# Performance work log

Measured on AMD Instinct MI355X. Metric: run time of the kernel, lower is better.

The kernel has to match this reference:

```python
import jax, jax.numpy as jnp
import numpy as np

ALPHA, BETA, GAMMA = 2.0, 2.0, 1.0
EPS = 1e-8  # torch F.cosine_similarity eps
B, T, D = 64, 1024, 256


def setup_inputs() -> dict:
    key = jax.random.key(0)
    k1, k2, k3 = jax.random.split(key, 3)
    f_v = jax.random.normal(k1, (B, T, D), dtype=jnp.float32)
    f_a = jax.random.normal(k2, (B, T, D), dtype=jnp.float32)
    labels = jax.random.randint(k3, (B,), 0, 2, dtype=jnp.int64)
    return {"f_v": f_v, "f_a": f_a, "labels": labels}


def _normalize(x):
    n = jnp.sqrt(jnp.sum(x * x, axis=-1, keepdims=True))
    return x / jnp.maximum(n, EPS)


def reference(f_v, f_a, labels):
    b, t, _ = f_v.shape
    vn = _normalize(f_v)  # [B,T,D]
    an = _normalize(f_a)  # [B,T,D]

    # --- per-timestep aligned-pair term ---
    cos_bt = jnp.sum(vn * an, axis=-1)  # [B,T] cosine sim
    d_bt = 1.0 - cos_bt                  # cosine distance
    pos_mask = (labels == 0).astype(f_v.dtype)[:, None]  # [B,1]
    neg_mask = 1.0 - pos_mask
    loss_pos = ALPHA * jnp.sum(d_bt * pos_mask)
    cnt_pos = jnp.sum(pos_mask) * t
    loss_neg = BETA * jnp.sum((1.0 - d_bt) * neg_mask)  # (1-d) == cos
    cnt_neg = jnp.sum(neg_mask) * t

    # --- cross-sample term: for i != j, (1 - mean_t d_ij) = mean_t cos(v_i_t, a_j_t) ---
    cross_cos = jnp.einsum('itd,jtd->ij', vn, an) / t  # [B,B] mean over T
    offdiag = 1.0 - jnp.eye(b, dtype=f_v.dtype)
    loss_neg = loss_neg + GAMMA * jnp.sum(cross_cos * offdiag)
    cnt_neg = cnt_neg + b * (b - 1)

    loss = jnp.where(cnt_pos > 0, loss_pos / jnp.maximum(cnt_pos, 1.0), 0.0)
    loss = loss + jnp.where(cnt_neg > 0, loss_neg / jnp.maximum(cnt_neg, 1.0), 0.0)
    return loss
```

## Files before the change

### kernel.cpp

```cpp
#include <hip/hip_runtime.h>

constexpr int Bn = 64;
constexpr int Tn = 1024;
constexpr int Dn = 256;

constexpr int TPB  = 256;
constexpr int NBLK = Tn;

using short8 = __attribute__((ext_vector_type(8))) short;
using f32x16 = __attribute__((ext_vector_type(16))) float;

__device__ __forceinline__ float dot4(const float4& a, const float4& b) {
    return a.x * b.x + a.y * b.y + a.z * b.z + a.w * b.w;
}

__device__ __forceinline__ unsigned int bfbits(float x) {
    unsigned int u = __builtin_bit_cast(unsigned int, x);
    return (u + 0x7FFFu + ((u >> 16) & 1u)) >> 16;
}
__device__ __forceinline__ unsigned int pack_bf2(float lo, float hi) {
    return bfbits(lo) | (bfbits(hi) << 16);
}

__global__ __launch_bounds__(TPB, 4)
void cmfm_main(const float* __restrict__ fv, const float* __restrict__ fa,
               const int* __restrict__ labels, float* __restrict__ acc)
{
    __shared__ __align__(16) unsigned int Vb[Bn * 64];
    __shared__ __align__(16) unsigned int Ab[Bn * 64];
    __shared__ float rvs[Bn], ras[Bn];
    __shared__ float wred[3][TPB / 64];

    const int tid  = threadIdx.x;
    const int row  = tid >> 2;
    const int q    = tid & 3;
    const int lane = tid & 63;
    const int wave = tid >> 6;

    const int lab = labels[row];
    const float4* __restrict__ fv4 = reinterpret_cast<const float4*>(fv);
    const float4* __restrict__ fa4 = reinterpret_cast<const float4*>(fa);

    const int t = blockIdx.x;
    const size_t base = ((size_t)row * Tn + t) * (Dn / 4);

    const int i0   = (wave >> 1) * 32;
    const int j0   = (wave & 1) * 32;
    const int mrow = lane & 31;
    const int half = lane >> 5;
    const int rsx  = mrow & 15;
    const unsigned vrb = (unsigned)(i0 + mrow) * 64;
    const unsigned arb = (unsigned)(j0 + mrow) * 64;

    const int wsx = row & 15;
    const unsigned wrb = (unsigned)row * 64;

    f32x16 C;
    #pragma unroll
    for (int r = 0; r < 16; ++r) C[r] = 0.f;

    float sqv = 0.f, sqa = 0.f, dva = 0.f;
    float rv = 0.f, ra = 0.f;

    #pragma unroll
    for (int h = 0; h < 2; ++h) {
        float4 v4[8], a4[8];
        #pragma unroll
        for (int k = 0; k < 8; ++k) v4[k] = fv4[base + q + 4 * (8 * h + k)];
        #pragma unroll
        for (int k = 0; k < 8; ++k) a4[k] = fa4[base + q + 4 * (8 * h + k)];

        #pragma unroll
        for (int k = 0; k < 8; ++k) {
            sqv += dot4(v4[k], v4[k]);
            sqa += dot4(a4[k], a4[k]);
            dva += dot4(v4[k], a4[k]);
        }

        #pragma unroll
        for (int k = 0; k < 8; ++k) {
            const int d4l  = q + 4 * k;
            const int slot = d4l >> 1;
            const unsigned idx = wrb + (unsigned)(((slot ^ wsx) << 2) + (d4l & 1) * 2);
            uint2 pv, pa;
            pv.x = pack_bf2(v4[k].x, v4[k].y); pv.y = pack_bf2(v4[k].z, v4[k].w);
            pa.x = pack_bf2(a4[k].x, a4[k].y); pa.y = pack_bf2(a4[k].z, a4[k].w);
            *reinterpret_cast<uint2*>(&Vb[idx]) = pv;
            *reinterpret_cast<uint2*>(&Ab[idx]) = pa;
        }

        if (h == 1) {
            sqv += __shfl_xor(sqv, 1); sqv += __shfl_xor(sqv, 2);
            sqa += __shfl_xor(sqa, 1); sqa += __shfl_xor(sqa, 2);
            dva += __shfl_xor(dva, 1); dva += __shfl_xor(dva, 2);
            rv = 1.f / fmaxf(sqrtf(sqv), 1e-8f);
            ra = 1.f / fmaxf(sqrtf(sqa), 1e-8f);
            if (q == 0) { rvs[row] = rv; ras[row] = ra; }
        }
        __syncthreads();

        #pragma unroll
        for (int s = 0; s < 8; ++s) {
            const int slotl = s * 2 + half;
            const short8 av = *reinterpret_cast<const short8*>(&Vb[vrb + ((slotl ^ rsx) << 2)]);
            const short8 bv = *reinterpret_cast<const short8*>(&Ab[arb + ((slotl ^ rsx) << 2)]);
            C = __builtin_amdgcn_mfma_f32_32x32x16_bf16(av, bv, C, 0, 0, 0);
        }
        if (h == 0) __syncthreads();
    }

    float pos_acc = 0.f, neg_acc = 0.f;
    if (q == 0) {
        const float cosd = dva * rv * ra;
        if (lab == 0) pos_acc = 1.f - cosd;
        else          neg_acc = cosd;
    }

    const float raj = ras[j0 + mrow];
    float od = 0.f;
    #pragma unroll
    for (int r = 0; r < 16; ++r) {
        const int ri = (r & 3) + 8 * (r >> 2) + 4 * half;
        float c = C[r];
        if (i0 == j0 && ri == mrow) c = 0.f;
        od += rvs[i0 + ri] * raj * c;
    }

    #pragma unroll
    for (int off = 1; off < 64; off <<= 1) {
        pos_acc += __shfl_xor(pos_acc, off);
        neg_acc += __shfl_xor(neg_acc, off);
        od      += __shfl_xor(od, off);
    }
    if (lane == 0) { wred[0][wave] = pos_acc; wred[1][wave] = neg_acc; wred[2][wave] = od; }
    __syncthreads();
    if (tid == 0) {
        float p = 0.f, n = 0.f, o = 0.f;
        #pragma unroll
        for (int w = 0; w < TPB / 64; ++w) { p += wred[0][w]; n += wred[1][w]; o += wred[2][w]; }
        atomicAdd(&acc[0],  p);
        atomicAdd(&acc[16], n);
        atomicAdd(&acc[32], o);
    }
}

__global__ void cmfm_final(const int* __restrict__ labels, const float* __restrict__ acc,
                           float* __restrict__ out) {
    if (threadIdx.x == 0) {
        int npos = 0;
        for (int i = 0; i < Bn; ++i) npos += (labels[i] == 0);
        const float pos_sum   = acc[0];
        const float neg_sum   = acc[16];
        const float cross_sum = acc[32];

        const float cnt_pos = (float)npos * (float)Tn;
        const float cnt_neg = (float)(Bn - npos) * (float)Tn + (float)Bn * (float)(Bn - 1);

        float loss = 0.f;
        if (npos > 0) loss += 2.0f * pos_sum / cnt_pos;
        loss += (2.0f * neg_sum + 1.0f * cross_sum / (float)Tn) / cnt_neg;
        out[0] = loss;
    }
}

extern "C" void kernel_launch(void* const* d_in, const int* in_sizes, int n_in,
                              void* d_out, int out_size, void* d_ws, size_t ws_size,
                              hipStream_t stream) {
    const float* fv     = (const float*)d_in[0];
    const float* fa     = (const float*)d_in[1];
    const int*   labels = (const int*)d_in[2];
    float* acc = (float*)d_ws;
    float* out = (float*)d_out;

    hipMemsetAsync(acc, 0, 64 * sizeof(float), stream);
    cmfm_main<<<NBLK, TPB, 0, stream>>>(fv, fa, labels, acc);
    cmfm_final<<<1, 64, 0, stream>>>(labels, acc, out);
}
```

Measured before the change: 161.0 us.

## Software-pipeline D-chunk loads and fold final reduction into main kernel

Splits the D dimension into four 64-wide chunks with double-buffered register prefetch, so global loads of the next chunk overlap the bf16 packing and MFMA work on the current one. Shared staging buffers are halved and the swizzle is adjusted to match. The separate finalize kernel is removed: the last block, found through an atomic ticket counter, computes the loss, and the positive-label count is derived inside each block. This trades one kernel launch for more barriers per block and a threadfence plus atomic counter.

Result: slower. 198.5 us (+23.3%).

```diff
diff --git a/kernel.cpp b/kernel.cpp
--- a/kernel.cpp
+++ b/kernel.cpp
@@ -24,12 +24,13 @@
 
 __global__ __launch_bounds__(TPB, 4)
 void cmfm_main(const float* __restrict__ fv, const float* __restrict__ fa,
-               const int* __restrict__ labels, float* __restrict__ acc)
+               const int* __restrict__ labels, float* __restrict__ acc,
+               float* __restrict__ out)
 {
-    __shared__ __align__(16) unsigned int Vb[Bn * 64];
-    __shared__ __align__(16) unsigned int Ab[Bn * 64];
+    __shared__ __align__(16) unsigned int Vb[Bn * 32];
+    __shared__ __align__(16) unsigned int Ab[Bn * 32];
     __shared__ float rvs[Bn], ras[Bn];
-    __shared__ float wred[3][TPB / 64];
+    __shared__ float wred[4][TPB / 64];
 
     const int tid  = threadIdx.x;
     const int row  = tid >> 2;
@@ -48,12 +49,12 @@
     const int j0   = (wave & 1) * 32;
     const int mrow = lane & 31;
     const int half = lane >> 5;
-    const int rsx  = mrow & 15;
-    const unsigned vrb = (unsigned)(i0 + mrow) * 64;
-    const unsigned arb = (unsigned)(j0 + mrow) * 64;
+    const int rsx  = mrow & 7;
+    const unsigned vrb = (unsigned)(i0 + mrow) * 32;
+    const unsigned arb = (unsigned)(j0 + mrow) * 32;
 
-    const int wsx = row & 15;
-    const unsigned wrb = (unsigned)row * 64;
+    const int wsx = row & 7;
+    const unsigned wrb = (unsigned)row * 32;
 
     f32x16 C;
     #pragma unroll
@@ -62,34 +63,43 @@
     float sqv = 0.f, sqa = 0.f, dva = 0.f;
     float rv = 0.f, ra = 0.f;
 
+    float4 va[2][4], ab4[2][4];
+
     #pragma unroll
-    for (int h = 0; h < 2; ++h) {
-        float4 v4[8], a4[8];
-        #pragma unroll
-        for (int k = 0; k < 8; ++k) v4[k] = fv4[base + q + 4 * (8 * h + k)];
-        #pragma unroll
-        for (int k = 0; k < 8; ++k) a4[k] = fa4[base + q + 4 * (8 * h + k)];
+    for (int k = 0; k < 4; ++k) va[0][k] = fv4[base + q + 4 * k];
+    #pragma unroll
+    for (int k = 0; k < 4; ++k) ab4[0][k] = fa4[base + q + 4 * k];
 
-        #pragma unroll
-        for (int k = 0; k < 8; ++k) {
-            sqv += dot4(v4[k], v4[k]);
-            sqa += dot4(a4[k], a4[k]);
-            dva += dot4(v4[k], a4[k]);
+    #pragma unroll
+    for (int qq = 0; qq < 4; ++qq) {
+        const int cur = qq & 1;
+        const int nxt = cur ^ 1;
+
+        if (qq < 3) {
+            #pragma unroll
+            for (int k = 0; k < 4; ++k) va[nxt][k]  = fv4[base + (qq + 1) * 16 + q + 4 * k];
+            #pragma unroll
+            for (int k = 0; k < 4; ++k) ab4[nxt][k] = fa4[base + (qq + 1) * 16 + q + 4 * k];
         }
 
         #pragma unroll
-        for (int k = 0; k < 8; ++k) {
+        for (int k = 0; k < 4; ++k) {
+            const float4 v = va[cur][k];
+            const float4 a = ab4[cur][k];
+            sqv += dot4(v, v);
+            sqa += dot4(a, a);
+            dva += dot4(v, a);
             const int d4l  = q + 4 * k;
             const int slot = d4l >> 1;
             const unsigned idx = wrb + (unsigned)(((slot ^ wsx) << 2) + (d4l & 1) * 2);
             uint2 pv, pa;
-            pv.x = pack_bf2(v4[k].x, v4[k].y); pv.y = pack_bf2(v4[k].z, v4[k].w);
-            pa.x = pack_bf2(a4[k].x, a4[k].y); pa.y = pack_bf2(a4[k].z, a4[k].w);
+            pv.x = pack_bf2(v.x, v.y); pv.y = pack_bf2(v.z, v.w);
+            pa.x = pack_bf2(a.x, a.y); pa.y = pack_bf2(a.z, a.w);
             *reinterpret_cast<uint2*>(&Vb[idx]) = pv;
             *reinterpret_cast<uint2*>(&Ab[idx]) = pa;
         }
 
-        if (h == 1) {
+        if (qq == 3) {
             sqv += __shfl_xor(sqv, 1); sqv += __shfl_xor(sqv, 2);
             sqa += __shfl_xor(sqa, 1); sqa += __shfl_xor(sqa, 2);
             dva += __shfl_xor(dva, 1); dva += __shfl_xor(dva, 2);
@@ -100,20 +110,20 @@
         __syncthreads();
 
         #pragma unroll
-        for (int s = 0; s < 8; ++s) {
+        for (int s = 0; s < 4; ++s) {
             const int slotl = s * 2 + half;
             const short8 av = *reinterpret_cast<const short8*>(&Vb[vrb + ((slotl ^ rsx) << 2)]);
             const short8 bv = *reinterpret_cast<const short8*>(&Ab[arb + ((slotl ^ rsx) << 2)]);
             C = __builtin_amdgcn_mfma_f32_32x32x16_bf16(av, bv, C, 0, 0, 0);
         }
-        if (h == 0) __syncthreads();
+        __syncthreads();
     }
 
-    float pos_acc = 0.f, neg_acc = 0.f;
+    float pos_acc = 0.f, neg_acc = 0.f, npos_i = 0.f;
     if (q == 0) {
         const float cosd = dva * rv * ra;
-        if (lab == 0) pos_acc = 1.f - cosd;
-        else          neg_acc = cosd;
+        if (lab == 0) { pos_acc = 1.f - cosd; npos_i = 1.f; }
+        else          { neg_acc = cosd; }
     }
 
     const float raj = ras[j0 + mrow];
@@ -131,35 +141,39 @@
         pos_acc += __shfl_xor(pos_acc, off);
         neg_acc += __shfl_xor(neg_acc, off);
         od      += __shfl_xor(od, off);
+        npos_i  += __shfl_xor(npos_i, off);
     }
-    if (lane == 0) { wred[0][wave] = pos_acc; wred[1][wave] = neg_acc; wred[2][wave] = od; }
+    if (lane == 0) {
+        wred[0][wave] = pos_acc; wred[1][wave] = neg_acc;
+        wred[2][wave] = od;      wred[3][wave] = npos_i;
+    }
     __syncthreads();
+
     if (tid == 0) {
-        float p = 0.f, n = 0.f, o = 0.f;
+        float p = 0.f, n = 0.f, o = 0.f, npf = 0.f;
         #pragma unroll
-        for (int w = 0; w < TPB / 64; ++w) { p += wred[0][w]; n += wred[1][w]; o += wred[2][w]; }
+        for (int w = 0; w < TPB / 64; ++w) {
+            p += wred[0][w]; n += wred[1][w]; o += wred[2][w]; npf += wred[3][w];
+        }
         atomicAdd(&acc[0],  p);
         atomicAdd(&acc[16], n);
         atomicAdd(&acc[32], o);
-    }
-}
-
-__global__ void cmfm_final(const int* __restrict__ labels, const float* __restrict__ acc,
-                           float* __restrict__ out) {
-    if (threadIdx.x == 0) {
-        int npos = 0;
-        for (int i = 0; i < Bn; ++i) npos += (labels[i] == 0);
-        const float pos_sum   = acc[0];
-        const float neg_sum   = acc[16];
-        const float cross_sum = acc[32];
-
-        const float cnt_pos = (float)npos * (float)Tn;
-        const float cnt_neg = (float)(Bn - npos) * (float)Tn + (float)Bn * (float)(Bn - 1);
-
-        float loss = 0.f;
-        if (npos > 0) loss += 2.0f * pos_sum / cnt_pos;
-        loss += (2.0f * neg_sum + 1.0f * cross_sum / (float)Tn) / cnt_neg;
-        out[0] = loss;
+        __threadfence();
+        int* ctr = reinterpret_cast<int*>(acc) + 48;
+        const int old = atomicAdd(ctr, 1);
+        if (old == NBLK - 1) {
+            __threadfence();
+            const float pos_sum   = atomicAdd(&acc[0],  0.f);
+            const float neg_sum   = atomicAdd(&acc[16], 0.f);
+            const float cross_sum = atomicAdd(&acc[32], 0.f);
+            const int   np        = (int)(npf + 0.5f);
+            const float cnt_pos = (float)np * (float)Tn;
+            const float cnt_neg = (float)(Bn - np) * (float)Tn + (float)Bn * (float)(Bn - 1);
+            float loss = 0.f;
+            if (np > 0) loss += 2.0f * pos_sum / cnt_pos;
+            loss += (2.0f * neg_sum + 1.0f * cross_sum / (float)Tn) / cnt_neg;
+            out[0] = loss;
+        }
     }
 }
 
@@ -173,6 +187,5 @@
     float* out = (float*)d_out;
 
     hipMemsetAsync(acc, 0, 64 * sizeof(float), stream);
-    cmfm_main<<<NBLK, TPB, 0, stream>>>(fv, fa, labels, acc);
-    cmfm_final<<<1, 64, 0, stream>>>(labels, acc, out);
+    cmfm_main<<<NBLK, TPB, 0, stream>>>(fv, fa, labels, acc, out);
 }
```

## Feed MFMA directly from registers with one-wave blocks per quadrant

Applied to the files above, without the earlier changes.

Each block becomes a single wave that handles one 32x32 quadrant of the cross-sample matrix at one timestep. It loads fp32 rows straight into registers, packs them to bf16 and feeds the MFMA without the shared-memory staging and barriers. Norms are exchanged with shuffles instead of LDS, and atomics are spread over 64 bins that the final kernel reduces. The cost is redundant global reads: each row is loaded by two quadrant blocks, doubling read traffic, which may rely on L2 hits.

New measurement: 272.9 us. 1.69x slower.

```diff
diff --git a/kernel.cpp b/kernel.cpp
--- a/kernel.cpp
+++ b/kernel.cpp
@@ -4,8 +4,10 @@
 constexpr int Tn = 1024;
 constexpr int Dn = 256;
 
-constexpr int TPB  = 256;
-constexpr int NBLK = Tn;
+constexpr int TPB   = 64;
+constexpr int QUADS = 4;
+constexpr int NBLK  = Tn * QUADS;
+constexpr int NBIN  = 64;
 
 using short8 = __attribute__((ext_vector_type(8))) short;
 using f32x16 = __attribute__((ext_vector_type(16))) float;
@@ -26,139 +28,108 @@
 void cmfm_main(const float* __restrict__ fv, const float* __restrict__ fa,
                const int* __restrict__ labels, float* __restrict__ acc)
 {
-    __shared__ __align__(16) unsigned int Vb[Bn * 64];
-    __shared__ __align__(16) unsigned int Ab[Bn * 64];
-    __shared__ float rvs[Bn], ras[Bn];
-    __shared__ float wred[3][TPB / 64];
+    const int lane = threadIdx.x;
+    const int bid  = blockIdx.x;
 
-    const int tid  = threadIdx.x;
-    const int row  = tid >> 2;
-    const int q    = tid & 3;
-    const int lane = tid & 63;
-    const int wave = tid >> 6;
-
-    const int lab = labels[row];
-    const float4* __restrict__ fv4 = reinterpret_cast<const float4*>(fv);
-    const float4* __restrict__ fa4 = reinterpret_cast<const float4*>(fa);
-
-    const int t = blockIdx.x;
-    const size_t base = ((size_t)row * Tn + t) * (Dn / 4);
-
-    const int i0   = (wave >> 1) * 32;
-    const int j0   = (wave & 1) * 32;
+    const int lid  = (bid & 7) * (NBLK / 8) + (bid >> 3);
+    const int t    = lid >> 2;
+    const int quad = lid & 3;
+    const int i0   = (quad >> 1) * 32;
+    const int j0   = (quad & 1) * 32;
     const int mrow = lane & 31;
     const int half = lane >> 5;
-    const int rsx  = mrow & 15;
-    const unsigned vrb = (unsigned)(i0 + mrow) * 64;
-    const unsigned arb = (unsigned)(j0 + mrow) * 64;
+    const bool diag = (i0 == j0);
 
-    const int wsx = row & 15;
-    const unsigned wrb = (unsigned)row * 64;
+    const float* __restrict__ vrow = fv + ((size_t)(i0 + mrow) * Tn + t) * Dn + 8 * half;
+    const float* __restrict__ arow = fa + ((size_t)(j0 + mrow) * Tn + t) * Dn + 8 * half;
 
     f32x16 C;
     #pragma unroll
     for (int r = 0; r < 16; ++r) C[r] = 0.f;
 
     float sqv = 0.f, sqa = 0.f, dva = 0.f;
-    float rv = 0.f, ra = 0.f;
 
     #pragma unroll
-    for (int h = 0; h < 2; ++h) {
-        float4 v4[8], a4[8];
-        #pragma unroll
-        for (int k = 0; k < 8; ++k) v4[k] = fv4[base + q + 4 * (8 * h + k)];
-        #pragma unroll
-        for (int k = 0; k < 8; ++k) a4[k] = fa4[base + q + 4 * (8 * h + k)];
+    for (int s = 0; s < 16; ++s) {
+        const float4 v0 = *reinterpret_cast<const float4*>(vrow + 16 * s);
+        const float4 v1 = *reinterpret_cast<const float4*>(vrow + 16 * s + 4);
+        const float4 a0 = *reinterpret_cast<const float4*>(arow + 16 * s);
+        const float4 a1 = *reinterpret_cast<const float4*>(arow + 16 * s + 4);
 
-        #pragma unroll
-        for (int k = 0; k < 8; ++k) {
-            sqv += dot4(v4[k], v4[k]);
-            sqa += dot4(a4[k], a4[k]);
-            dva += dot4(v4[k], a4[k]);
-        }
+        sqv += dot4(v0, v0) + dot4(v1, v1);
+        sqa += dot4(a0, a0) + dot4(a1, a1);
+        if (diag) dva += dot4(v0, a0) + dot4(v1, a1);
 
-        #pragma unroll
-        for (int k = 0; k < 8; ++k) {
-            const int d4l  = q + 4 * k;
-            const int slot = d4l >> 1;
-            const unsigned idx = wrb + (unsigned)(((slot ^ wsx) << 2) + (d4l & 1) * 2);
-            uint2 pv, pa;
-            pv.x = pack_bf2(v4[k].x, v4[k].y); pv.y = pack_bf2(v4[k].z, v4[k].w);
-            pa.x = pack_bf2(a4[k].x, a4[k].y); pa.y = pack_bf2(a4[k].z, a4[k].w);
-            *reinterpret_cast<uint2*>(&Vb[idx]) = pv;
-            *reinterpret_cast<uint2*>(&Ab[idx]) = pa;
-        }
+        union { short8 s8; uint4 u4; } av, bv;
+        av.u4.x = pack_bf2(v0.x, v0.y); av.u4.y = pack_bf2(v0.z, v0.w);
+        av.u4.z = pack_bf2(v1.x, v1.y); av.u4.w = pack_bf2(v1.z, v1.w);
+        bv.u4.x = pack_bf2(a0.x, a0.y); bv.u4.y = pack_bf2(a0.z, a0.w);
+        bv.u4.z = pack_bf2(a1.x, a1.y); bv.u4.w = pack_bf2(a1.z, a1.w);
 
-        if (h == 1) {
-            sqv += __shfl_xor(sqv, 1); sqv += __shfl_xor(sqv, 2);
-            sqa += __shfl_xor(sqa, 1); sqa += __shfl_xor(sqa, 2);
-            dva += __shfl_xor(dva, 1); dva += __shfl_xor(dva, 2);
-            rv = 1.f / fmaxf(sqrtf(sqv), 1e-8f);
-            ra = 1.f / fmaxf(sqrtf(sqa), 1e-8f);
-            if (q == 0) { rvs[row] = rv; ras[row] = ra; }
-        }
-        __syncthreads();
-
-        #pragma unroll
-        for (int s = 0; s < 8; ++s) {
-            const int slotl = s * 2 + half;
-            const short8 av = *reinterpret_cast<const short8*>(&Vb[vrb + ((slotl ^ rsx) << 2)]);
-            const short8 bv = *reinterpret_cast<const short8*>(&Ab[arb + ((slotl ^ rsx) << 2)]);
-            C = __builtin_amdgcn_mfma_f32_32x32x16_bf16(av, bv, C, 0, 0, 0);
-        }
-        if (h == 0) __syncthreads();
+        C = __builtin_amdgcn_mfma_f32_32x32x16_bf16(av.s8, bv.s8, C, 0, 0, 0);
     }
 
-    float pos_acc = 0.f, neg_acc = 0.f;
-    if (q == 0) {
+    sqv += __shfl_xor(sqv, 32);
+    sqa += __shfl_xor(sqa, 32);
+    const float rv = 1.f / fmaxf(sqrtf(sqv), 1e-8f);
+    const float ra = 1.f / fmaxf(sqrtf(sqa), 1e-8f);
+
+    float pos = 0.f, neg = 0.f;
+    if (diag) {
+        dva += __shfl_xor(dva, 32);
         const float cosd = dva * rv * ra;
-        if (lab == 0) pos_acc = 1.f - cosd;
-        else          neg_acc = cosd;
+        const int lab = labels[i0 + mrow];
+        if (half == 0) {
+            if (lab == 0) pos = 1.f - cosd;
+            else          neg = cosd;
+        }
     }
 
-    const float raj = ras[j0 + mrow];
     float od = 0.f;
     #pragma unroll
     for (int r = 0; r < 16; ++r) {
         const int ri = (r & 3) + 8 * (r >> 2) + 4 * half;
+        const float rvi = __shfl(rv, ri);
         float c = C[r];
-        if (i0 == j0 && ri == mrow) c = 0.f;
-        od += rvs[i0 + ri] * raj * c;
+        if (diag && ri == mrow) c = 0.f;
+        od += rvi * ra * c;
     }
 
     #pragma unroll
     for (int off = 1; off < 64; off <<= 1) {
-        pos_acc += __shfl_xor(pos_acc, off);
-        neg_acc += __shfl_xor(neg_acc, off);
-        od      += __shfl_xor(od, off);
+        pos += __shfl_xor(pos, off);
+        neg += __shfl_xor(neg, off);
+        od  += __shfl_xor(od, off);
     }
-    if (lane == 0) { wred[0][wave] = pos_acc; wred[1][wave] = neg_acc; wred[2][wave] = od; }
-    __syncthreads();
-    if (tid == 0) {
-        float p = 0.f, n = 0.f, o = 0.f;
-        #pragma unroll
-        for (int w = 0; w < TPB / 64; ++w) { p += wred[0][w]; n += wred[1][w]; o += wred[2][w]; }
-        atomicAdd(&acc[0],  p);
-        atomicAdd(&acc[16], n);
-        atomicAdd(&acc[32], o);
+    if (lane == 0) {
+        float* bin = acc + (size_t)(bid & (NBIN - 1)) * 4;
+        atomicAdd(bin + 0, pos);
+        atomicAdd(bin + 1, neg);
+        atomicAdd(bin + 2, od);
     }
 }
 
 __global__ void cmfm_final(const int* __restrict__ labels, const float* __restrict__ acc,
                            float* __restrict__ out) {
-    if (threadIdx.x == 0) {
-        int npos = 0;
-        for (int i = 0; i < Bn; ++i) npos += (labels[i] == 0);
-        const float pos_sum   = acc[0];
-        const float neg_sum   = acc[16];
-        const float cross_sum = acc[32];
-
-        const float cnt_pos = (float)npos * (float)Tn;
-        const float cnt_neg = (float)(Bn - npos) * (float)Tn + (float)Bn * (float)(Bn - 1);
-
+    const int l = threadIdx.x;
+    float p = acc[l * 4 + 0];
+    float n = acc[l * 4 + 1];
+    float o = acc[l * 4 + 2];
+    float npf = (labels[l] == 0) ? 1.f : 0.f;
+    #pragma unroll
+    for (int off = 1; off < 64; off <<= 1) {
+        p += __shfl_xor(p, off);
+        n += __shfl_xor(n, off);
+        o += __shfl_xor(o, off);
+        npf += __shfl_xor(npf, off);
+    }
+    if (l == 0) {
+        const int np = (int)(npf + 0.5f);
+        const float cnt_pos = (float)np * (float)Tn;
+        const float cnt_neg = (float)(Bn - np) * (float)Tn + (float)Bn * (float)(Bn - 1);
         float loss = 0.f;
-        if (npos > 0) loss += 2.0f * pos_sum / cnt_pos;
-        loss += (2.0f * neg_sum + 1.0f * cross_sum / (float)Tn) / cnt_neg;
+        if (np > 0) loss += 2.0f * p / cnt_pos;
+        loss += (2.0f * n + 1.0f * o / (float)Tn) / cnt_neg;
         out[0] = loss;
     }
 }
@@ -172,7 +143,7 @@
     float* acc = (float*)d_ws;
     float* out = (float*)d_out;
 
-    hipMemsetAsync(acc, 0, 64 * sizeof(float), stream);
+    hipMemsetAsync(acc, 0, NBIN * 4 * sizeof(float), stream);
     cmfm_main<<<NBLK, TPB, 0, stream>>>(fv, fa, labels, acc);
     cmfm_final<<<1, 64, 0, stream>>>(labels, acc, out);
 }
```
